# Kernel tuning notes

Hardware: AMD Instinct MI355X
Metric: run time of the kernel (lower is better)

The kernel has to match this reference:

```python
import jax, jax.numpy as jnp
import numpy as np

N = 800_000
D = 128
S = 64
EPS = 1e-16  # matches torch_geometric softmax denominator epsilon


def setup_inputs() -> dict:
    key = jax.random.key(0)
    k1, k2, k3 = jax.random.split(key, 3)
    x = jax.random.normal(k1, (N, D), dtype=jnp.float32)
    batch = jnp.sort(jax.random.randint(k2, (N,), 0, S, dtype=jnp.int64))
    gate_W = jax.random.normal(k3, (D, 1), dtype=jnp.float32) * (1.0 / np.sqrt(D))
    gate_b = jnp.zeros((1,), dtype=jnp.float32)
    return {"x": x, "batch": batch, "size": S, "gate_W": gate_W, "gate_b": gate_b}


def reference(x, batch, size, gate_W, gate_b):
    # gate = gate_nn(x).view(-1, 1)  -> [N]
    gate = (x @ gate_W + gate_b)[:, 0]
    # segment-wise numerically-stable softmax over nodes of each graph
    seg_max = jax.ops.segment_max(gate, batch, num_segments=size,
                                  indices_are_sorted=True)
    # guard empty segments (-inf max)
    seg_max = jnp.where(jnp.isfinite(seg_max), seg_max, 0.0)
    g = jnp.exp(gate - seg_max[batch])
    denom = jax.ops.segment_sum(g, batch, num_segments=size,
                                indices_are_sorted=True)
    gate_sm = g / (denom[batch] + EPS)          # [N]
    # weighted scatter-add pooling: out[s] = sum_{i in seg s} gate_i * x_i
    out = jax.ops.segment_sum(gate_sm[:, None] * x, batch, num_segments=size,
                              indices_are_sorted=True)  # [S, D]
    return out, gate_sm[:, None]
```

## Files before the change

kernel.cpp:

```cpp
#include <hip/hip_runtime.h>
#include <hip/hip_bf16.h>
#include <math.h>

#define D 128
#define EPS 1e-16f
#define K_SLOTS 4
#define REC_STRIDE 132
#define NBLK_A 2048
#define THR_A 256
#define NWV (NBLK_A * THR_A / 64)
#define NREC (NWV * K_SLOTS)
#define NBLK_R 2048
#define RB (NREC / NBLK_R)

__device__ __forceinline__ unsigned f2o(float f) {
    unsigned u = __float_as_uint(f);
    return (u & 0x80000000u) ? ~u : (u | 0x80000000u);
}
__device__ __forceinline__ float o2f(unsigned o) {
    return (o & 0x80000000u) ? __uint_as_float(o & 0x7fffffffu) : __uint_as_float(~o);
}
__device__ __forceinline__ float bcast0(float v) {
    return __uint_as_float(__builtin_amdgcn_readfirstlane(__float_as_uint(v)));
}

__global__ void k_init(unsigned* __restrict__ segMkey, float* __restrict__ denomAcc,
                       float* __restrict__ outAcc, int S) {
    const int t = blockIdx.x * blockDim.x + threadIdx.x;
    const int stride = gridDim.x * blockDim.x;
    for (int i = t; i < S; i += stride) { segMkey[i] = 0x007FFFFFu; denomAcc[i] = 0.f; }
    for (int i = t; i < S * D; i += stride) outAcc[i] = 0.f;
}

__global__ __launch_bounds__(256) void k_fused(const float* __restrict__ x,
        const int* __restrict__ batch,
        const float* __restrict__ W,
        const float* __restrict__ bptr,
        float* __restrict__ gate,
        float* __restrict__ recs,
        unsigned* __restrict__ segMkey,
        int N, int chunk) {
    const int lane = threadIdx.x & 63;
    const int sub  = lane & 31;
    const int h    = lane >> 5;
    const int wv   = (blockIdx.x * blockDim.x + threadIdx.x) >> 6;
    const int i0   = wv * chunk;
    const int i1   = min(N, i0 + chunk);
    float* myrec = recs + (size_t)wv * K_SLOTS * REC_STRIDE;
    if (i0 >= i1) {
        if (lane == 0)
            for (int s = 0; s < K_SLOTS; ++s)
                ((int*)(myrec + (size_t)s * REC_STRIDE))[0] = -1;
        return;
    }

    const float4 w = ((const float4*)W)[sub];
    const float bias = bptr[0];

    float4 acc = make_float4(0.f, 0.f, 0.f, 0.f);
    float m = -INFINITY, l = 0.f;
    int cur = batch[i0];
    int cnt = 0;

    auto flush = [&]() {
        acc.x += __shfl_xor(acc.x, 32);
        acc.y += __shfl_xor(acc.y, 32);
        acc.z += __shfl_xor(acc.z, 32);
        acc.w += __shfl_xor(acc.w, 32);
        float* r = myrec + min(cnt, K_SLOTS - 1) * REC_STRIDE;
        if (lane == 0) { ((int*)r)[0] = cur; r[1] = m; r[2] = l; }
        if (h == 0) ((float4*)(r + 4))[sub] = acc;
        if (lane == 0) atomicMax(&segMkey[cur], f2o(m));
        ++cnt;
        acc = make_float4(0.f, 0.f, 0.f, 0.f); m = -INFINITY; l = 0.f;
    };

    auto one = [&](int b, float gs, int hr, float4 xv) {
        if (b != cur) { flush(); cur = b; }
        const float m2 = fmaxf(m, gs);
        const float s  = __expf(m - m2);
        const float e  = __expf(gs - m2);
        l = l * s + e;
        const float es = (h == hr) ? e : 0.f;
        acc.x = acc.x * s + es * xv.x;
        acc.y = acc.y * s + es * xv.y;
        acc.z = acc.z * s + es * xv.z;
        acc.w = acc.w * s + es * xv.w;
        m = m2;
    };

    const int n = i1 - i0;
    const int npair = n >> 1;

    if (npair > 0) {
        float4 xc = ((const float4*)(x + (size_t)i0 * D))[lane];
        int b0c = batch[i0], b1c = batch[i0 + 1];
        float4 xn = xc; int b0n = b0c, b1n = b1c;
        if (npair > 1) {
            xn = ((const float4*)(x + (size_t)(i0 + 2) * D))[lane];
            b0n = batch[i0 + 2]; b1n = batch[i0 + 3];
        }
        for (int p = 0; p < npair; ++p) {
            float4 x2 = xn; int b02 = b0n, b12 = b1n;
            if (p + 2 < npair) {
                const int ir = i0 + 2 * (p + 2);
                x2 = ((const float4*)(x + (size_t)ir * D))[lane];
                b02 = batch[ir]; b12 = batch[ir + 1];
            }
            const int i = i0 + 2 * p;
            float pd = xc.x * w.x + xc.y * w.y + xc.z * w.z + xc.w * w.w;
            pd += __shfl_xor(pd, 1);
            pd += __shfl_xor(pd, 2);
            pd += __shfl_xor(pd, 4);
            pd += __shfl_xor(pd, 8);
            pd += __shfl_xor(pd, 16);
            const float g  = pd + bias;
            const float go = __shfl_xor(g, 32);
            const float g0 = bcast0(g);
            const float g1 = bcast0(go);
            if (sub == 0) gate[i + h] = g;

            if (b0c == cur && b1c == cur) {
                const float m2 = fmaxf(fmaxf(m, g0), g1);
                const float s  = __expf(m - m2);
                const float e  = __expf(g - m2);
                l = l * s + __expf(g0 - m2) + __expf(g1 - m2);
                acc.x = acc.x * s + e * xc.x;
                acc.y = acc.y * s + e * xc.y;
                acc.z = acc.z * s + e * xc.z;
                acc.w = acc.w * s + e * xc.w;
                m = m2;
            } else {
                one(b0c, g0, 0, xc);
                one(b1c, g1, 1, xc);
            }
            xc = xn; b0c = b0n; b1c = b1n;
            xn = x2; b0n = b02; b1n = b12;
        }
    }
    if (n & 1) {
        const int i = i1 - 1;
        float4 xt = ((const float4*)(x + (size_t)i * D))[sub];
        float pd = xt.x * w.x + xt.y * w.y + xt.z * w.z + xt.w * w.w;
        pd += __shfl_xor(pd, 1);
        pd += __shfl_xor(pd, 2);
        pd += __shfl_xor(pd, 4);
        pd += __shfl_xor(pd, 8);
        pd += __shfl_xor(pd, 16);
        const float gs = bcast0(pd + bias);
        if (lane == 0) gate[i] = gs;
        one(batch[i], gs, 0, xt);
    }
    flush();
    if (lane == 0)
        for (int s = min(cnt, K_SLOTS); s < K_SLOTS; ++s)
            ((int*)(myrec + (size_t)s * REC_STRIDE))[0] = -1;
}

__global__ __launch_bounds__(128) void k_acc(const float* __restrict__ recs,
        const unsigned* __restrict__ segMkey,
        float* __restrict__ denomAcc, float* __restrict__ outAcc) {
    const int j  = threadIdx.x;
    const int r0 = blockIdx.x * RB;
    float a = 0.f, dl = 0.f;
    int curseg = -1;

    const float* rec0 = recs + (size_t)r0 * REC_STRIDE;
    int   seg_n = ((const int*)rec0)[0];
    float m_n   = rec0[1];
    float l_n   = rec0[2];
    float v_n   = rec0[4 + j];

    for (int r = r0; r < r0 + RB; ++r) {
        const int   seg = seg_n;
        const float mm  = m_n;
        const float ll  = l_n;
        const float v   = v_n;
        const int rn = min(r + 1, NREC - 1);
        const float* recn = recs + (size_t)rn * REC_STRIDE;
        seg_n = ((const int*)recn)[0];
        m_n   = recn[1];
        l_n   = recn[2];
        v_n   = recn[4 + j];

        if (seg < 0) continue;
        if (seg != curseg) {
            if (curseg >= 0) {
                atomicAdd(&outAcc[(size_t)curseg * D + j], a);
                if (j == 0) atomicAdd(&denomAcc[curseg], dl);
            }
            curseg = seg; a = 0.f; dl = 0.f;
        }
        const float sc = __expf(mm - o2f(segMkey[seg]));
        a += sc * v;
        if (j == 0) dl += sc * ll;
    }
    if (curseg >= 0) {
        atomicAdd(&outAcc[(size_t)curseg * D + j], a);
        if (j == 0) atomicAdd(&denomAcc[curseg], dl);
    }
}

__global__ __launch_bounds__(256) void k_final(const float* __restrict__ gate,
                        const int* __restrict__ batch,
                        const unsigned* __restrict__ segMkey,
                        const float* __restrict__ denomAcc,
                        const float* __restrict__ outAcc,
                        float* __restrict__ out, float* __restrict__ gate_sm,
                        int N, int SD) {
    const int t = blockIdx.x * blockDim.x + threadIdx.x;
    const int stride = gridDim.x * blockDim.x;
    for (int i = t; i < SD; i += stride)
        out[i] = outAcc[i] / (denomAcc[i >> 7] + EPS);
    const int n4 = N >> 2;
    for (int q = t; q < n4; q += stride) {
        const int4   b4 = ((const int4*)batch)[q];
        const float4 g4 = ((const float4*)gate)[q];
        float4 r;
        r.x = __expf(g4.x - o2f(segMkey[b4.x])) / (denomAcc[b4.x] + EPS);
        r.y = __expf(g4.y - o2f(segMkey[b4.y])) / (denomAcc[b4.y] + EPS);
        r.z = __expf(g4.z - o2f(segMkey[b4.z])) / (denomAcc[b4.z] + EPS);
        r.w = __expf(g4.w - o2f(segMkey[b4.w])) / (denomAcc[b4.w] + EPS);
        ((float4*)gate_sm)[q] = r;
    }
    for (int i = (n4 << 2) + t; i < N; i += stride) {
        const int b = batch[i];
        gate_sm[i] = __expf(gate[i] - o2f(segMkey[b])) / (denomAcc[b] + EPS);
    }
}

extern "C" void kernel_launch(void* const* d_in, const int* in_sizes, int n_in,
                              void* d_out, int out_size, void* d_ws, size_t ws_size,
                              hipStream_t stream) {
    const float* x      = (const float*)d_in[0];
    const int*   batch  = (const int*)d_in[1];
    const float* gate_W = (const float*)d_in[3];
    const float* gate_b = (const float*)d_in[4];

    const int N = in_sizes[0] / D;
    const int S = (out_size - N) / D;

    float* out     = (float*)d_out;
    float* gate_sm = (float*)d_out + (size_t)S * D;

    float*    gate     = (float*)d_ws;
    unsigned* segMkey  = (unsigned*)(gate + N);
    float*    denomAcc = (float*)(segMkey + S);
    float*    outAcc   = denomAcc + S;
    size_t off = ((size_t)(N + 2 * S + S * D) + 3) & ~(size_t)3;
    float*    recs     = (float*)d_ws + off;

    int chunk = (N + NWV - 1) / NWV;
    chunk = (chunk + 1) & ~1;

    k_init<<<64, 256, 0, stream>>>(segMkey, denomAcc, outAcc, S);
    k_fused<<<NBLK_A, THR_A, 0, stream>>>(x, batch, gate_W, gate_b, gate, recs, segMkey, N, chunk);
    k_acc<<<NBLK_R, 128, 0, stream>>>(recs, segMkey, denomAcc, outAcc);
    k_final<<<1024, 256, 0, stream>>>(gate, batch, segMkey, denomAcc, outAcc, out, gate_sm, N, S * D);
}
```

Baseline: 617.8 us.

## Use nontemporal loads/stores for streaming x and gate_sm, skip rescale when max unchanged

Streams x with nontemporal float4 loads and writes gate_sm with nontemporal stores, so single-use data does not pollute the cache. Adds an occupancy hint of 8 waves per SIMD to the fused kernel's launch bounds. In the same-segment pair path, computes the two exponentials with one exp plus a lane shuffle and skips the rescale exp and multiplies when the running max is unchanged. The extra branch could cause divergence, and the occupancy hint may force register spilling.

```diff
diff --git a/kernel.cpp b/kernel.cpp
--- a/kernel.cpp
+++ b/kernel.cpp
@@ -13,6 +13,8 @@
 #define NBLK_R 2048
 #define RB (NREC / NBLK_R)
 
+typedef float vf4 __attribute__((ext_vector_type(4)));
+
 __device__ __forceinline__ unsigned f2o(float f) {
     unsigned u = __float_as_uint(f);
     return (u & 0x80000000u) ? ~u : (u | 0x80000000u);
@@ -22,6 +24,14 @@
 }
 __device__ __forceinline__ float bcast0(float v) {
     return __uint_as_float(__builtin_amdgcn_readfirstlane(__float_as_uint(v)));
+}
+__device__ __forceinline__ float4 ld_nt4(const float4* p) {
+    vf4 v = __builtin_nontemporal_load((const vf4*)p);
+    return make_float4(v.x, v.y, v.z, v.w);
+}
+__device__ __forceinline__ void st_nt4(float4* p, float4 f) {
+    vf4 v = {f.x, f.y, f.z, f.w};
+    __builtin_nontemporal_store(v, (vf4*)p);
 }
 
 __global__ void k_init(unsigned* __restrict__ segMkey, float* __restrict__ denomAcc,
@@ -32,7 +42,7 @@
     for (int i = t; i < S * D; i += stride) outAcc[i] = 0.f;
 }
 
-__global__ __launch_bounds__(256) void k_fused(const float* __restrict__ x,
+__global__ __launch_bounds__(256, 8) void k_fused(const float* __restrict__ x,
         const int* __restrict__ batch,
         const float* __restrict__ W,
         const float* __restrict__ bptr,
@@ -93,18 +103,18 @@
     const int npair = n >> 1;
 
     if (npair > 0) {
-        float4 xc = ((const float4*)(x + (size_t)i0 * D))[lane];
+        float4 xc = ld_nt4(((const float4*)(x + (size_t)i0 * D)) + lane);
         int b0c = batch[i0], b1c = batch[i0 + 1];
         float4 xn = xc; int b0n = b0c, b1n = b1c;
         if (npair > 1) {
-            xn = ((const float4*)(x + (size_t)(i0 + 2) * D))[lane];
+            xn = ld_nt4(((const float4*)(x + (size_t)(i0 + 2) * D)) + lane);
             b0n = batch[i0 + 2]; b1n = batch[i0 + 3];
         }
         for (int p = 0; p < npair; ++p) {
             float4 x2 = xn; int b02 = b0n, b12 = b1n;
             if (p + 2 < npair) {
                 const int ir = i0 + 2 * (p + 2);
-                x2 = ((const float4*)(x + (size_t)ir * D))[lane];
+                x2 = ld_nt4(((const float4*)(x + (size_t)ir * D)) + lane);
                 b02 = batch[ir]; b12 = batch[ir + 1];
             }
             const int i = i0 + 2 * p;
@@ -122,14 +132,23 @@
 
             if (b0c == cur && b1c == cur) {
                 const float m2 = fmaxf(fmaxf(m, g0), g1);
-                const float s  = __expf(m - m2);
                 const float e  = __expf(g - m2);
-                l = l * s + __expf(g0 - m2) + __expf(g1 - m2);
-                acc.x = acc.x * s + e * xc.x;
-                acc.y = acc.y * s + e * xc.y;
-                acc.z = acc.z * s + e * xc.z;
-                acc.w = acc.w * s + e * xc.w;
-                m = m2;
+                const float eo = __shfl_xor(e, 32);
+                if (m2 == m) {
+                    l = l + e + eo;
+                    acc.x += e * xc.x;
+                    acc.y += e * xc.y;
+                    acc.z += e * xc.z;
+                    acc.w += e * xc.w;
+                } else {
+                    const float s = __expf(m - m2);
+                    l = l * s + e + eo;
+                    acc.x = acc.x * s + e * xc.x;
+                    acc.y = acc.y * s + e * xc.y;
+                    acc.z = acc.z * s + e * xc.z;
+                    acc.w = acc.w * s + e * xc.w;
+                    m = m2;
+                }
             } else {
                 one(b0c, g0, 0, xc);
                 one(b1c, g1, 1, xc);
@@ -140,7 +159,7 @@
     }
     if (n & 1) {
         const int i = i1 - 1;
-        float4 xt = ((const float4*)(x + (size_t)i * D))[sub];
+        float4 xt = ld_nt4(((const float4*)(x + (size_t)i * D)) + sub);
         float pd = xt.x * w.x + xt.y * w.y + xt.z * w.z + xt.w * w.w;
         pd += __shfl_xor(pd, 1);
         pd += __shfl_xor(pd, 2);
@@ -221,7 +240,7 @@
         r.y = __expf(g4.y - o2f(segMkey[b4.y])) / (denomAcc[b4.y] + EPS);
         r.z = __expf(g4.z - o2f(segMkey[b4.z])) / (denomAcc[b4.z] + EPS);
         r.w = __expf(g4.w - o2f(segMkey[b4.w])) / (denomAcc[b4.w] + EPS);
-        ((float4*)gate_sm)[q] = r;
+        st_nt4(((float4*)gate_sm) + q, r);
     }
     for (int i = (n4 << 2) + t; i < N; i += stride) {
         const int b = batch[i];
```

Measured after the change: 575.1 us. -6.9%, faster.
